# Optimization experiments

Measured on AMD Instinct MI355X. Metric: run time of the kernel, lower is better.

Reference implementation:

```python
import jax, jax.numpy as jnp
import numpy as np

N_NODES = 100000
N_EDGES = 1600000
NODE_DIM = 128
HIDDEN_DIM = 128


def _sage_conv(x, src, dst, deg_inv, W_l, W_r, b):
    # PyG SAGEConv (aggr='mean', root_weight=True):
    #   out = lin_l(mean_{j in N(i)} x_j) + lin_r(x_i)
    msgs = x[src]                                             # [E, d_in] gather
    agg = jax.ops.segment_sum(msgs, dst, num_segments=N_NODES)  # [N, d_in]
    mean = agg * deg_inv[:, None]
    return mean @ W_l + x @ W_r + b


def setup_inputs() -> dict:
    key = jax.random.key(0)
    ks = jax.random.split(key, 9)
    x = jax.random.normal(ks[0], (N_NODES, NODE_DIM), dtype=jnp.float32)
    edge_index = jax.random.randint(ks[1], (2, N_EDGES), 0, N_NODES, dtype=jnp.int32)
    t = jnp.zeros((1,), dtype=jnp.float32)

    def glorot(k, fan_in, fan_out):
        s = (6.0 / (fan_in + fan_out)) ** 0.5
        return jax.random.uniform(k, (fan_in, fan_out), jnp.float32, -s, s)

    return {
        "t": t,
        "x": x,
        "edge_index": edge_index,
        "W1_l": glorot(ks[2], NODE_DIM, HIDDEN_DIM),
        "W1_r": glorot(ks[3], NODE_DIM, HIDDEN_DIM),
        "b1": jnp.zeros((HIDDEN_DIM,), jnp.float32),
        "W2_l": glorot(ks[4], HIDDEN_DIM, HIDDEN_DIM),
        "W2_r": glorot(ks[5], HIDDEN_DIM, HIDDEN_DIM),
        "b2": jnp.zeros((HIDDEN_DIM,), jnp.float32),
        "W3_l": glorot(ks[6], HIDDEN_DIM, NODE_DIM),
        "W3_r": glorot(ks[7], HIDDEN_DIM, NODE_DIM),
        "b3": jnp.zeros((NODE_DIM,), jnp.float32),
    }


def reference(t, x, edge_index, W1_l, W1_r, b1, W2_l, W2_r, b2, W3_l, W3_r, b3):
    src, dst = edge_index[0], edge_index[1]
    deg = jax.ops.segment_sum(jnp.ones((N_EDGES,), x.dtype), dst, num_segments=N_NODES)
    deg_inv = jnp.where(deg > 0, 1.0 / jnp.maximum(deg, 1.0), 0.0)

    h = jax.nn.relu(_sage_conv(x, src, dst, deg_inv, W1_l, W1_r, b1))
    h = jax.nn.relu(_sage_conv(h, src, dst, deg_inv, W2_l, W2_r, b2))
    dx_dt = _sage_conv(h, src, dst, deg_inv, W3_l, W3_r, b3)
    return dx_dt
```

## Files before the change

### kernel.cpp

```cpp
#include <hip/hip_runtime.h>

#define NN   100000
#define NE   1600000
#define DIM  128
#define NBKT 391
#define EPB  16384
#define NBLK 98
#define NTILES (NN / 16)

typedef short          s16x8 __attribute__((ext_vector_type(8)));
typedef unsigned short u16x8 __attribute__((ext_vector_type(8)));
typedef float          f32x4 __attribute__((ext_vector_type(4)));

__device__ __forceinline__ unsigned short f2b(float f) {
    unsigned u = __float_as_uint(f);
    unsigned r = ((u >> 16) & 1u) + 0x7FFFu;
    return (unsigned short)((u + r) >> 16);
}
__device__ __forceinline__ float b2f(unsigned short h) {
    return __uint_as_float(((unsigned)h) << 16);
}

__global__ void k_cast_x(const float* __restrict__ x, unsigned short* __restrict__ xb) {
    int i = blockIdx.x * blockDim.x + threadIdx.x;
    const float4* xp = (const float4*)x;
    float4 v = xp[i];
    ushort4 o;
    o.x = f2b(v.x); o.y = f2b(v.y); o.z = f2b(v.z); o.w = f2b(v.w);
    ((ushort4*)xb)[i] = o;
}

__global__ void k_hist2(const int* __restrict__ dst, int* __restrict__ hist) {
    __shared__ int lh[NBKT];
    int t = threadIdx.x, b = blockIdx.x;
    for (int j = t; j < NBKT; j += 256) lh[j] = 0;
    __syncthreads();
    int base = b * EPB;
    int end = base + EPB; if (end > NE) end = NE;
    for (int i = base + t; i < end; i += 256) atomicAdd(&lh[dst[i] >> 8], 1);
    __syncthreads();
    for (int j = t; j < NBKT; j += 256) hist[j * NBLK + b] = lh[j];
}

__global__ void k_scanrow(int* __restrict__ hist, int* __restrict__ row_total) {
    __shared__ int sh[128];
    int k = blockIdx.x, t = threadIdx.x;
    int v = (t < NBLK) ? hist[k * NBLK + t] : 0;
    sh[t] = v;
    __syncthreads();
    for (int off = 1; off < 128; off <<= 1) {
        int a = (t >= off) ? sh[t - off] : 0;
        __syncthreads();
        sh[t] += a;
        __syncthreads();
    }
    if (t < NBLK) hist[k * NBLK + t] = sh[t] - v;
    if (t == 127) row_total[k] = sh[127];
}

__global__ void k_scanbkt(const int* __restrict__ row_total, int* __restrict__ bbase) {
    __shared__ int sh[512];
    int t = threadIdx.x;
    int v = (t < NBKT) ? row_total[t] : 0;
    sh[t] = v;
    __syncthreads();
    for (int off = 1; off < 512; off <<= 1) {
        int a = (t >= off) ? sh[t - off] : 0;
        __syncthreads();
        sh[t] += a;
        __syncthreads();
    }
    if (t < NBKT) bbase[t] = sh[t] - v;
    if (t == NBKT) bbase[NBKT] = NE;
}

__global__ void k_bin2(const int* __restrict__ src, const int* __restrict__ dst,
                       const int* __restrict__ hist, const int* __restrict__ bbase,
                       int* __restrict__ binned) {
    __shared__ int s_base[NBKT];
    __shared__ int s_cnt[NBKT];
    int t = threadIdx.x, b = blockIdx.x;
    for (int j = t; j < NBKT; j += 256) {
        s_base[j] = bbase[j] + hist[j * NBLK + b];
        s_cnt[j] = 0;
    }
    __syncthreads();
    int base = b * EPB;
    int end = base + EPB; if (end > NE) end = NE;
    for (int i = base + t; i < end; i += 256) {
        int d = dst[i];
        int k = d >> 8;
        int w = (src[i] << 8) | (d & 255);
        int lpos = atomicAdd(&s_cnt[k], 1);
        binned[s_base[k] + lpos] = w;
    }
}

__global__ void k_build(const int* __restrict__ binned,
                        const int* __restrict__ bucket_base,
                        int* __restrict__ csr,
                        int* __restrict__ row_start, int* __restrict__ deg,
                        float* __restrict__ deg_inv) {
    __shared__ int s_deg[256], s_scan[256], s_cur[256];
    __shared__ int stage[8192];
    int b = blockIdx.x, t = threadIdx.x;
    int base = bucket_base[b], end = bucket_base[b + 1];
    int cnt = end - base;
    s_deg[t] = 0;
    __syncthreads();
    for (int i = t; i < cnt; i += 256)
        atomicAdd(&s_deg[binned[base + i] & 255], 1);
    __syncthreads();
    s_scan[t] = s_deg[t];
    __syncthreads();
    for (int off = 1; off < 256; off <<= 1) {
        int a = (t >= off) ? s_scan[t - off] : 0;
        __syncthreads();
        s_scan[t] += a;
        __syncthreads();
    }
    int excl = s_scan[t] - s_deg[t];
    s_cur[t] = excl;
    int node = b * 256 + t;
    if (node < NN) {
        int d = s_deg[t];
        row_start[node] = base + excl;
        deg[node]       = d;
        deg_inv[node]   = (d > 0) ? 1.0f / (float)d : 0.0f;
    }
    __syncthreads();
    for (int i = t; i < cnt; i += 256) {
        int w = binned[base + i];
        int pos = atomicAdd(&s_cur[w & 255], 1);
        int s = w >> 8;
        if (pos < 8192) stage[pos] = s;
        else            csr[base + pos] = s;
    }
    __syncthreads();
    int m = cnt < 8192 ? cnt : 8192;
    for (int i = t; i < m; i += 256) csr[base + i] = stage[i];
}

__global__ void k_castw(const float* __restrict__ W1l, const float* __restrict__ W1r,
                        const float* __restrict__ W2l, const float* __restrict__ W2r,
                        const float* __restrict__ W3l, const float* __restrict__ W3r,
                        unsigned short* __restrict__ Wt1, unsigned short* __restrict__ Wt2,
                        unsigned short* __restrict__ Wt3) {
    int i = blockIdx.x * blockDim.x + threadIdx.x;
    int L = i >> 15;
    int rem = i & 32767;
    int n = rem >> 8;
    int k = rem & 255;
    const float* Wl = (L == 0) ? W1l : (L == 1) ? W2l : W3l;
    const float* Wr = (L == 0) ? W1r : (L == 1) ? W2r : W3r;
    unsigned short* Wt = (L == 0) ? Wt1 : (L == 1) ? Wt2 : Wt3;
    float v = (k < 128) ? Wl[k * 128 + n] : Wr[(k - 128) * 128 + n];
    Wt[n * 256 + k] = f2b(v);
}

__global__ void k_gather(const unsigned short* __restrict__ feat,
                         const int* __restrict__ row_start, const int* __restrict__ deg,
                         const float* __restrict__ deg_inv, const int* __restrict__ csr,
                         unsigned short* __restrict__ mean) {
    int lane = threadIdx.x & 63;
    int wv   = threadIdx.x >> 6;
    int n    = blockIdx.x * 4 + wv;
    int q = lane >> 4, c = lane & 15;
    int base = row_start[n];
    int d    = deg[n];
    float acc0[8], acc1[8], acc2[8], acc3[8];
#pragma unroll
    for (int t = 0; t < 8; t++) { acc0[t] = 0.f; acc1[t] = 0.f; acc2[t] = 0.f; acc3[t] = 0.f; }
    const u16x8* fp = (const u16x8*)feat;
    int j = q;
    for (; j + 12 < d; j += 16) {
        int s0 = csr[base + j];
        int s1 = csr[base + j + 4];
        int s2 = csr[base + j + 8];
        int s3 = csr[base + j + 12];
        u16x8 v0 = fp[s0 * 16 + c];
        u16x8 v1 = fp[s1 * 16 + c];
        u16x8 v2 = fp[s2 * 16 + c];
        u16x8 v3 = fp[s3 * 16 + c];
#pragma unroll
        for (int t = 0; t < 8; t++) {
            acc0[t] += b2f(v0[t]); acc1[t] += b2f(v1[t]);
            acc2[t] += b2f(v2[t]); acc3[t] += b2f(v3[t]);
        }
    }
    for (; j + 4 < d; j += 8) {
        int s0 = csr[base + j];
        int s1 = csr[base + j + 4];
        u16x8 v0 = fp[s0 * 16 + c];
        u16x8 v1 = fp[s1 * 16 + c];
#pragma unroll
        for (int t = 0; t < 8; t++) { acc0[t] += b2f(v0[t]); acc1[t] += b2f(v1[t]); }
    }
    if (j < d) {
        int s0 = csr[base + j];
        u16x8 v0 = fp[s0 * 16 + c];
#pragma unroll
        for (int t = 0; t < 8; t++) acc0[t] += b2f(v0[t]);
    }
#pragma unroll
    for (int t = 0; t < 8; t++) acc0[t] += (acc1[t] + acc2[t]) + acc3[t];
#pragma unroll
    for (int t = 0; t < 8; t++) {
        acc0[t] += __shfl_xor(acc0[t], 16, 64);
        acc0[t] += __shfl_xor(acc0[t], 32, 64);
    }
    if (q == 0) {
        float s = deg_inv[n];
        u16x8 o;
#pragma unroll
        for (int t = 0; t < 8; t++) o[t] = f2b(acc0[t] * s);
        ((u16x8*)mean)[n * 16 + c] = o;
    }
}

template <int MODE>
__global__ void __launch_bounds__(512)
k_lin(const unsigned short* __restrict__ meanb,
      const unsigned short* __restrict__ hb,
      const unsigned short* __restrict__ Wt,
      const float* __restrict__ bias, void* __restrict__ out) {
    __shared__ s16x8 sW[4096];
    int t = threadIdx.x;
    const s16x8* wp = (const s16x8*)Wt;
#pragma unroll
    for (int it = 0; it < 8; it++) {
        int ci = it * 512 + t;
        int frag = ci >> 6, ln = ci & 63;
        int mt = frag >> 3, kt = frag & 7;
        int m = mt * 16 + (ln & 15);
        int kc = kt * 4 + (ln >> 4);
        sW[ci] = wp[m * 32 + kc];
    }
    __syncthreads();

    int lane = t & 63;
    int wv   = t >> 6;
    int tile = blockIdx.x * 8 + wv;
    if (tile >= NTILES) return;
    int n0 = tile * 16;
    int q = lane >> 4, c = lane & 15;
    const s16x8* mp = (const s16x8*)meanb;
    const s16x8* hp = (const s16x8*)hb;
    int row = n0 + c;
    s16x8 B[8];
#pragma unroll
    for (int kt = 0; kt < 4; kt++) B[kt] = mp[row * 16 + kt * 4 + q];
#pragma unroll
    for (int kt = 0; kt < 4; kt++) B[4 + kt] = hp[row * 16 + kt * 4 + q];
    const f32x4* bp = (const f32x4*)bias;
#pragma unroll
    for (int mt = 0; mt < 8; mt++) {
        f32x4 acc = {0.f, 0.f, 0.f, 0.f};
#pragma unroll
        for (int kt = 0; kt < 8; kt++)
            acc = __builtin_amdgcn_mfma_f32_16x16x32_bf16(sW[(mt * 8 + kt) * 64 + lane],
                                                          B[kt], acc, 0, 0, 0);
        f32x4 bv = bp[mt * 4 + q];
        int node = n0 + c;
        if (MODE == 0) {
            ushort4 o;
            float v0 = acc[0] + bv[0]; if (v0 < 0.f) v0 = 0.f;
            float v1 = acc[1] + bv[1]; if (v1 < 0.f) v1 = 0.f;
            float v2 = acc[2] + bv[2]; if (v2 < 0.f) v2 = 0.f;
            float v3 = acc[3] + bv[3]; if (v3 < 0.f) v3 = 0.f;
            o.x = f2b(v0); o.y = f2b(v1); o.z = f2b(v2); o.w = f2b(v3);
            ((ushort4*)out)[node * 32 + mt * 4 + q] = o;
        } else {
            f32x4 v;
#pragma unroll
            for (int r = 0; r < 4; r++) v[r] = acc[r] + bv[r];
            ((f32x4*)out)[node * 32 + mt * 4 + q] = v;
        }
    }
}

extern "C" void kernel_launch(void* const* d_in, const int* in_sizes, int n_in,
                              void* d_out, int out_size, void* d_ws, size_t ws_size,
                              hipStream_t stream) {
    const float* x   = (const float*)d_in[1];
    const int*   ei  = (const int*)d_in[2];
    const int*   src = ei;
    const int*   dst = ei + NE;
    const float* W1l = (const float*)d_in[3];
    const float* W1r = (const float*)d_in[4];
    const float* b1  = (const float*)d_in[5];
    const float* W2l = (const float*)d_in[6];
    const float* W2r = (const float*)d_in[7];
    const float* b2  = (const float*)d_in[8];
    const float* W3l = (const float*)d_in[9];
    const float* W3r = (const float*)d_in[10];
    const float* b3  = (const float*)d_in[11];

    char* w = (char*)d_ws;
    auto carve = [&](size_t bytes) {
        void* p = (void*)w;
        w += (bytes + 255) & ~(size_t)255;
        return p;
    };
    int*   row_start = (int*)carve(NN * 4);
    int*   deg       = (int*)carve(NN * 4);
    float* deg_inv   = (float*)carve(NN * 4);
    int*   hist      = (int*)carve((size_t)NBKT * NBLK * 4);
    int*   row_total = (int*)carve(NBKT * 4);
    int*   bbase     = (int*)carve((NBKT + 1) * 4);
    int*   csr       = (int*)carve((size_t)NE * 4);
    unsigned short* Wt1 = (unsigned short*)carve(128 * 256 * 2);
    unsigned short* Wt2 = (unsigned short*)carve(128 * 256 * 2);
    unsigned short* Wt3 = (unsigned short*)carve(128 * 256 * 2);
    unsigned short* xb    = (unsigned short*)carve((size_t)NN * DIM * 2);
    unsigned short* meanb = (unsigned short*)carve((size_t)NN * DIM * 2);
    unsigned short* h1b   = (unsigned short*)carve((size_t)NN * DIM * 2);
    unsigned short* h2b   = xb;
    int*   binned    = (int*)meanb;

    k_cast_x<<<NN * DIM / 4 / 256, 256, 0, stream>>>(x, xb);
    k_hist2<<<NBLK, 256, 0, stream>>>(dst, hist);
    k_scanrow<<<NBKT, 128, 0, stream>>>(hist, row_total);
    k_scanbkt<<<1, 512, 0, stream>>>(row_total, bbase);
    k_bin2<<<NBLK, 256, 0, stream>>>(src, dst, hist, bbase, binned);
    k_build<<<NBKT, 256, 0, stream>>>(binned, bbase, csr, row_start, deg, deg_inv);
    k_castw<<<3 * 128 * 256 / 256, 256, 0, stream>>>(W1l, W1r, W2l, W2r, W3l, W3r,
                                                     Wt1, Wt2, Wt3);

    const int GB = NN / 4;
    const int LB = (NTILES + 7) / 8;

    k_gather<<<GB, 256, 0, stream>>>(xb, row_start, deg, deg_inv, csr, meanb);
    k_lin<0><<<LB, 512, 0, stream>>>(meanb, xb, Wt1, b1, (void*)h1b);
    k_gather<<<GB, 256, 0, stream>>>(h1b, row_start, deg, deg_inv, csr, meanb);
    k_lin<0><<<LB, 512, 0, stream>>>(meanb, h1b, Wt2, b2, (void*)h2b);
    k_gather<<<GB, 256, 0, stream>>>(h2b, row_start, deg, deg_inv, csr, meanb);
    k_lin<1><<<LB, 512, 0, stream>>>(meanb, h2b, Wt3, b3, d_out);
}
```

Before: 478.0 us.

## Merge x cast, histogram and weight cast into one prep kernel; shrink gather unroll

Combines the x bf16 cast, the destination histogram and the weight transpose-cast into a single launch that dispatches on block index, removing two kernel launches and letting the three independent jobs overlap. Separately, the gather kernel drops its 4-way unrolled edge loop and keeps only the 2-way loop, which lowers register pressure but leaves fewer loads in flight per thread. These are two unrelated changes bundled together.

New measurement: 451.6 us. 1.06x faster.

```diff
diff --git a/kernel.cpp b/kernel.cpp
--- a/kernel.cpp
+++ b/kernel.cpp
@@ -7,6 +7,8 @@
 #define EPB  16384
 #define NBLK 98
 #define NTILES (NN / 16)
+#define CASTB 12500
+#define CWB   384
 
 typedef short          s16x8 __attribute__((ext_vector_type(8)));
 typedef unsigned short u16x8 __attribute__((ext_vector_type(8)));
@@ -21,25 +23,41 @@
     return __uint_as_float(((unsigned)h) << 16);
 }
 
-__global__ void k_cast_x(const float* __restrict__ x, unsigned short* __restrict__ xb) {
-    int i = blockIdx.x * blockDim.x + threadIdx.x;
-    const float4* xp = (const float4*)x;
-    float4 v = xp[i];
-    ushort4 o;
-    o.x = f2b(v.x); o.y = f2b(v.y); o.z = f2b(v.z); o.w = f2b(v.w);
-    ((ushort4*)xb)[i] = o;
-}
-
-__global__ void k_hist2(const int* __restrict__ dst, int* __restrict__ hist) {
+__global__ void k_prep(const float* __restrict__ x, unsigned short* __restrict__ xb,
+                       const int* __restrict__ dst, int* __restrict__ hist,
+                       const float* __restrict__ W1l, const float* __restrict__ W1r,
+                       const float* __restrict__ W2l, const float* __restrict__ W2r,
+                       const float* __restrict__ W3l, const float* __restrict__ W3r,
+                       unsigned short* __restrict__ Wt1, unsigned short* __restrict__ Wt2,
+                       unsigned short* __restrict__ Wt3) {
     __shared__ int lh[NBKT];
     int t = threadIdx.x, b = blockIdx.x;
-    for (int j = t; j < NBKT; j += 256) lh[j] = 0;
-    __syncthreads();
-    int base = b * EPB;
-    int end = base + EPB; if (end > NE) end = NE;
-    for (int i = base + t; i < end; i += 256) atomicAdd(&lh[dst[i] >> 8], 1);
-    __syncthreads();
-    for (int j = t; j < NBKT; j += 256) hist[j * NBLK + b] = lh[j];
+    if (b < NBLK) {
+        for (int j = t; j < NBKT; j += 256) lh[j] = 0;
+        __syncthreads();
+        int base = b * EPB;
+        int end = base + EPB; if (end > NE) end = NE;
+        for (int i = base + t; i < end; i += 256) atomicAdd(&lh[dst[i] >> 8], 1);
+        __syncthreads();
+        for (int j = t; j < NBKT; j += 256) hist[j * NBLK + b] = lh[j];
+    } else if (b < NBLK + CASTB) {
+        int i = (b - NBLK) * 256 + t;
+        float4 v = ((const float4*)x)[i];
+        ushort4 o;
+        o.x = f2b(v.x); o.y = f2b(v.y); o.z = f2b(v.z); o.w = f2b(v.w);
+        ((ushort4*)xb)[i] = o;
+    } else {
+        int i = (b - NBLK - CASTB) * 256 + t;
+        int L = i >> 15;
+        int rem = i & 32767;
+        int n = rem >> 8;
+        int k = rem & 255;
+        const float* Wl = (L == 0) ? W1l : (L == 1) ? W2l : W3l;
+        const float* Wr = (L == 0) ? W1r : (L == 1) ? W2r : W3r;
+        unsigned short* Wt = (L == 0) ? Wt1 : (L == 1) ? Wt2 : Wt3;
+        float v = (k < 128) ? Wl[k * 128 + n] : Wr[(k - 128) * 128 + n];
+        Wt[n * 256 + k] = f2b(v);
+    }
 }
 
 __global__ void k_scanrow(int* __restrict__ hist, int* __restrict__ row_total) {
@@ -141,23 +159,6 @@
     for (int i = t; i < m; i += 256) csr[base + i] = stage[i];
 }
 
-__global__ void k_castw(const float* __restrict__ W1l, const float* __restrict__ W1r,
-                        const float* __restrict__ W2l, const float* __restrict__ W2r,
-                        const float* __restrict__ W3l, const float* __restrict__ W3r,
-                        unsigned short* __restrict__ Wt1, unsigned short* __restrict__ Wt2,
-                        unsigned short* __restrict__ Wt3) {
-    int i = blockIdx.x * blockDim.x + threadIdx.x;
-    int L = i >> 15;
-    int rem = i & 32767;
-    int n = rem >> 8;
-    int k = rem & 255;
-    const float* Wl = (L == 0) ? W1l : (L == 1) ? W2l : W3l;
-    const float* Wr = (L == 0) ? W1r : (L == 1) ? W2r : W3r;
-    unsigned short* Wt = (L == 0) ? Wt1 : (L == 1) ? Wt2 : Wt3;
-    float v = (k < 128) ? Wl[k * 128 + n] : Wr[(k - 128) * 128 + n];
-    Wt[n * 256 + k] = f2b(v);
-}
-
 __global__ void k_gather(const unsigned short* __restrict__ feat,
                          const int* __restrict__ row_start, const int* __restrict__ deg,
                          const float* __restrict__ deg_inv, const int* __restrict__ csr,
@@ -168,26 +169,11 @@
     int q = lane >> 4, c = lane & 15;
     int base = row_start[n];
     int d    = deg[n];
-    float acc0[8], acc1[8], acc2[8], acc3[8];
-#pragma unroll
-    for (int t = 0; t < 8; t++) { acc0[t] = 0.f; acc1[t] = 0.f; acc2[t] = 0.f; acc3[t] = 0.f; }
+    float acc0[8], acc1[8];
+#pragma unroll
+    for (int t = 0; t < 8; t++) { acc0[t] = 0.0f; acc1[t] = 0.0f; }
     const u16x8* fp = (const u16x8*)feat;
     int j = q;
-    for (; j + 12 < d; j += 16) {
-        int s0 = csr[base + j];
-        int s1 = csr[base + j + 4];
-        int s2 = csr[base + j + 8];
-        int s3 = csr[base + j + 12];
-        u16x8 v0 = fp[s0 * 16 + c];
-        u16x8 v1 = fp[s1 * 16 + c];
-        u16x8 v2 = fp[s2 * 16 + c];
-        u16x8 v3 = fp[s3 * 16 + c];
-#pragma unroll
-        for (int t = 0; t < 8; t++) {
-            acc0[t] += b2f(v0[t]); acc1[t] += b2f(v1[t]);
-            acc2[t] += b2f(v2[t]); acc3[t] += b2f(v3[t]);
-        }
-    }
     for (; j + 4 < d; j += 8) {
         int s0 = csr[base + j];
         int s1 = csr[base + j + 4];
@@ -203,7 +189,7 @@
         for (int t = 0; t < 8; t++) acc0[t] += b2f(v0[t]);
     }
 #pragma unroll
-    for (int t = 0; t < 8; t++) acc0[t] += (acc1[t] + acc2[t]) + acc3[t];
+    for (int t = 0; t < 8; t++) acc0[t] += acc1[t];
 #pragma unroll
     for (int t = 0; t < 8; t++) {
         acc0[t] += __shfl_xor(acc0[t], 16, 64);
@@ -318,14 +304,13 @@
     unsigned short* h2b   = xb;
     int*   binned    = (int*)meanb;
 
-    k_cast_x<<<NN * DIM / 4 / 256, 256, 0, stream>>>(x, xb);
-    k_hist2<<<NBLK, 256, 0, stream>>>(dst, hist);
+    k_prep<<<NBLK + CASTB + CWB, 256, 0, stream>>>(x, xb, dst, hist,
+                                                   W1l, W1r, W2l, W2r, W3l, W3r,
+                                                   Wt1, Wt2, Wt3);
     k_scanrow<<<NBKT, 128, 0, stream>>>(hist, row_total);
     k_scanbkt<<<1, 512, 0, stream>>>(row_total, bbase);
     k_bin2<<<NBLK, 256, 0, stream>>>(src, dst, hist, bbase, binned);
     k_build<<<NBKT, 256, 0, stream>>>(binned, bbase, csr, row_start, deg, deg_inv);
-    k_castw<<<3 * 128 * 256 / 256, 256, 0, stream>>>(W1l, W1r, W2l, W2r, W3l, W3r,
-                                                     Wt1, Wt2, Wt3);
 
     const int GB = NN / 4;
     const int LB = (NTILES + 7) / 8;
```
